# Kernel optimization log

Hardware: AMD Instinct MI355X
Metric: run time of the kernel (lower is better)

## Reference

```python
import jax, jax.numpy as jnp
import numpy as np

EMBED_DIM = 512
NUM_TYPES = 26
PER_TYPE = 128
NUM_CODES = NUM_TYPES * PER_TYPE
COMMIT = 0.25
TEMP = 0.07
N_TOKENS = 32768
SAMPLED_PER_TYPE = int(0.1 * PER_TYPE)  # 12


def _normalize(v, axis=-1):
    # matches F.normalize(p=2) with eps clamp
    return v / jnp.clip(jnp.linalg.norm(v, axis=axis, keepdims=True), 1e-12)


def setup_inputs() -> dict:
    key = jax.random.key(0)
    k1, k2, k3, k4 = jax.random.split(key, 4)
    x = jax.random.normal(k1, (N_TOKENS, EMBED_DIM), jnp.float32)
    Q = jax.random.randint(k2, (N_TOKENS,), 0, NUM_TYPES)
    initrange = 1.0 / EMBED_DIM
    emb = jax.random.uniform(k3, (NUM_CODES, EMBED_DIM), jnp.float32, -initrange, initrange)
    emb = _normalize(emb)  # mirrors _initialize_embeddings
    # deterministic stand-in for torch.randperm(num_per_type)[:sampled_num]
    perm = jax.random.permutation(k4, PER_TYPE)[:SAMPLED_PER_TYPE]
    sampled_indices = (jnp.arange(NUM_TYPES)[:, None] * PER_TYPE + perm[None, :]).reshape(-1)
    return {"x": x, "embeddings": emb, "Q": Q, "sampled_indices": sampled_indices}


def _code_indices(xn, embeddings, Q):
    # full [N, num_codes] squared distances, then select the 128-code slab of
    # each token's PTM type and argmin within it (equivalent to the per-type loop)
    d = ((xn ** 2).sum(-1, keepdims=True)
         + (embeddings ** 2).sum(-1)[None, :]
         - 2.0 * (xn @ embeddings.T))                      # [N, NUM_CODES]
    d = d.reshape(xn.shape[0], NUM_TYPES, PER_TYPE)
    d_sel = jnp.take_along_axis(d, Q[:, None, None], axis=1)[:, 0, :]  # [N, PER_TYPE]
    return jnp.argmin(d_sel, axis=1) + Q * PER_TYPE


def _uniform_loss(embeddings, sampled_indices):
    ne = _normalize(embeddings)
    se = ne[sampled_indices]                               # [S, D]
    sim = se @ se.T                                        # [S, S]
    labels = sampled_indices // PER_TYPE
    pos = (labels[None, :] == labels[:, None]).astype(jnp.float32)
    S = sampled_indices.shape[0]
    eye = jnp.eye(S, dtype=bool)
    sim = jnp.where(eye, -jnp.inf, sim)
    sim_exp = jnp.exp(sim / TEMP)                          # exp(-inf) = 0 kills diagonal
    sum_exp = sim_exp.sum(axis=1)
    pos_sum = (sim_exp * pos).sum(axis=1)
    return -jnp.log(pos_sum / sum_exp).mean()


def reference(x, embeddings, Q, sampled_indices):
    xn = _normalize(x)
    idx = _code_indices(xn, embeddings, Q)
    quantized = _normalize(embeddings[idx])
    q_latent = jnp.mean((quantized - jax.lax.stop_gradient(xn)) ** 2)
    e_latent = jnp.mean((xn - jax.lax.stop_gradient(quantized)) ** 2)
    loss = q_latent + COMMIT * e_latent
    uloss = _uniform_loss(embeddings, sampled_indices)
    out = xn + jax.lax.stop_gradient(quantized - xn)       # straight-through
    return out, loss, uloss, idx
```

## Files before the change

### kernel.cpp

```cpp
#include <hip/hip_runtime.h>
#include <math.h>

#define NTOK   32768
#define DIM    512
#define NTYPES 26
#define PT     128
#define NCODES 3328
#define NSAMP  312
#define INV_TEMP (1.0f / 0.07f)
#define MAXTILES 24

typedef __attribute__((ext_vector_type(8))) short short8;
typedef __attribute__((ext_vector_type(4))) float floatx4;

__device__ __forceinline__ void f2bf2(float f, unsigned short& h, unsigned short& l) {
    unsigned u = __float_as_uint(f);
    unsigned hb = (u + 0x7fffu + ((u >> 16) & 1u)) >> 16;
    h = (unsigned short)hb;
    float hf = __uint_as_float(hb << 16);
    float r = f - hf;
    unsigned u2 = __float_as_uint(r);
    l = (unsigned short)((u2 + 0x7fffu + ((u2 >> 16) & 1u)) >> 16);
}

__device__ __forceinline__ void cvt8(float4 a, float4 b, short8& h, short8& l) {
    union { short8 v; unsigned short u[8]; } H, L;
    f2bf2(a.x, H.u[0], L.u[0]); f2bf2(a.y, H.u[1], L.u[1]);
    f2bf2(a.z, H.u[2], L.u[2]); f2bf2(a.w, H.u[3], L.u[3]);
    f2bf2(b.x, H.u[4], L.u[4]); f2bf2(b.y, H.u[5], L.u[5]);
    f2bf2(b.z, H.u[6], L.u[6]); f2bf2(b.w, H.u[7], L.u[7]);
    h = H.v; l = L.v;
}

__device__ __forceinline__ void stage2(const unsigned short* g, unsigned short* l) {
    __builtin_amdgcn_global_load_lds((const __attribute__((address_space(1))) void*)g,
                                     (__attribute__((address_space(3))) void*)l, 16, 0, 0);
    __builtin_amdgcn_global_load_lds((const __attribute__((address_space(1))) void*)(g + 512),
                                     (__attribute__((address_space(3))) void*)(l + 512), 16, 0, 0);
}

__global__ __launch_bounds__(256) void k_emb(const float* __restrict__ emb,
                                             unsigned short* __restrict__ Bhg,
                                             unsigned short* __restrict__ Blg,
                                             float* __restrict__ sume,
                                             float* __restrict__ rinv,
                                             int* __restrict__ counts,
                                             float* __restrict__ accg) {
    int tid = threadIdx.x;
    if (blockIdx.x == 0) {
        if (tid < NTYPES) counts[tid] = 0;
        if (tid == 32) accg[0] = 0.0f;
        if (tid == 33) accg[1] = 0.0f;
    }
    int wv = tid >> 6, lane = tid & 63;
    int c = blockIdx.x * 4 + wv;
    const float4* row = (const float4*)(emb + (size_t)c * DIM);
    float4 v0 = row[lane * 2], v1 = row[lane * 2 + 1];
    float s = v0.x*v0.x + v0.y*v0.y + v0.z*v0.z + v0.w*v0.w
            + v1.x*v1.x + v1.y*v1.y + v1.z*v1.z + v1.w*v1.w;
    for (int m = 32; m; m >>= 1) s += __shfl_xor(s, m);
    if (lane == 0) {
        sume[c] = s;
        rinv[c] = 1.0f / fmaxf(sqrtf(s), 1e-12f);
    }
    union { short8 v; unsigned short u[8]; } hh, ll;
    f2bf2(v0.x, hh.u[0], ll.u[0]); f2bf2(v0.y, hh.u[1], ll.u[1]);
    f2bf2(v0.z, hh.u[2], ll.u[2]); f2bf2(v0.w, hh.u[3], ll.u[3]);
    f2bf2(v1.x, hh.u[4], ll.u[4]); f2bf2(v1.y, hh.u[5], ll.u[5]);
    f2bf2(v1.z, hh.u[6], ll.u[6]); f2bf2(v1.w, hh.u[7], ll.u[7]);
    int qq  = c >> 7;
    int n   = c & 127;
    int ni  = n >> 4, lcc = n & 15;
    int ks2 = lane >> 2, q4d = lane & 3;
    size_t dst = (size_t)qq * (PT * DIM)
               + (size_t)(((ks2 * 8 + ni) * 64 + q4d * 16 + lcc) * 8);
    *(short8*)(Bhg + dst) = hh.v;
    *(short8*)(Blg + dst) = ll.v;
}

__global__ __launch_bounds__(256) void k_hist(const int* __restrict__ Q,
                                              int* __restrict__ counts,
                                              int* __restrict__ rank) {
    __shared__ int lbin[NTYPES];
    __shared__ int lbase[NTYPES];
    int tid = threadIdx.x;
    if (tid < NTYPES) lbin[tid] = 0;
    __syncthreads();
    int t = blockIdx.x * 256 + tid;
    int qt = Q[t];
    int lr = atomicAdd(&lbin[qt], 1);
    __syncthreads();
    if (tid < NTYPES) lbase[tid] = atomicAdd(&counts[tid], lbin[tid]);
    __syncthreads();
    rank[t] = lbase[qt] + lr;
}

__global__ __launch_bounds__(256) void k_scatter(const int* __restrict__ Q,
                                                 const int* __restrict__ counts,
                                                 const int* __restrict__ rank,
                                                 int* __restrict__ order,
                                                 int* __restrict__ offsg) {
    __shared__ int offs[NTYPES];
    int tid = threadIdx.x;
    if (tid == 0) {
        int a = 0;
        for (int i = 0; i < NTYPES; i++) {
            offs[i] = a;
            if (blockIdx.x == 0) offsg[i] = a;
            a += counts[i];
        }
        if (blockIdx.x == 0) offsg[NTYPES] = a;
    }
    __syncthreads();
    int t = blockIdx.x * 256 + tid;
    order[offs[Q[t]] + rank[t]] = t;
}

#define KSTEP(S, NSTR, AC, AF, DOSTAGE)                                          \
  {                                                                              \
    __builtin_amdgcn_sched_barrier(0);                                           \
    asm volatile("s_waitcnt vmcnt(" NSTR ")" ::: "memory");                      \
    __builtin_amdgcn_s_barrier();                                                \
    __builtin_amdgcn_sched_barrier(0);                                           \
    if (DOSTAGE) {                                                               \
      stage2(bhg + ((S) + 2) * 4096 + stoff, &Bls[((S) + 2) % 3][0][ldoff]);     \
      stage2(blg + ((S) + 2) * 4096 + stoff, &Bls[((S) + 2) % 3][1][ldoff]);     \
      AF[0] = *(const float4*)(ap0 + ((S) + 2) * 32);                            \
      AF[1] = *(const float4*)(ap0 + ((S) + 2) * 32 + 4);                        \
      AF[2] = *(const float4*)(ap1 + ((S) + 2) * 32);                            \
      AF[3] = *(const float4*)(ap1 + ((S) + 2) * 32 + 4);                        \
    }                                                                            \
    __builtin_amdgcn_sched_barrier(0);                                           \
    {                                                                            \
      float4 r0a = AC[0], r0b = AC[1], r1a = AC[2], r1b = AC[3];                 \
      ps0 = fmaf(r0a.x, r0a.x, fmaf(r0a.y, r0a.y, fmaf(r0a.z, r0a.z, fmaf(r0a.w, r0a.w, ps0)))); \
      ps0 = fmaf(r0b.x, r0b.x, fmaf(r0b.y, r0b.y, fmaf(r0b.z, r0b.z, fmaf(r0b.w, r0b.w, ps0)))); \
      ps1 = fmaf(r1a.x, r1a.x, fmaf(r1a.y, r1a.y, fmaf(r1a.z, r1a.z, fmaf(r1a.w, r1a.w, ps1)))); \
      ps1 = fmaf(r1b.x, r1b.x, fmaf(r1b.y, r1b.y, fmaf(r1b.z, r1b.z, fmaf(r1b.w, r1b.w, ps1)))); \
      short8 ah0, al0, ah1, al1;                                                 \
      cvt8(r0a, r0b, ah0, al0);                                                  \
      cvt8(r1a, r1b, ah1, al1);                                                  \
      short8 bhf[4], blf[4];                                                     \
      _Pragma("unroll")                                                          \
      for (int ni = 0; ni < 4; ni++) {                                           \
        bhf[ni] = *(const short8*)&Bls[(S) % 3][0][(wn4 + ni) * 512 + lane8];    \
        blf[ni] = *(const short8*)&Bls[(S) % 3][1][(wn4 + ni) * 512 + lane8];    \
      }                                                                          \
      _Pragma("unroll")                                                          \
      for (int ni = 0; ni < 4; ni++) {                                           \
        acc[0][ni] = __builtin_amdgcn_mfma_f32_16x16x32_bf16(ah0, bhf[ni], acc[0][ni], 0, 0, 0); \
        acc[0][ni] = __builtin_amdgcn_mfma_f32_16x16x32_bf16(ah0, blf[ni], acc[0][ni], 0, 0, 0); \
        acc[0][ni] = __builtin_amdgcn_mfma_f32_16x16x32_bf16(al0, bhf[ni], acc[0][ni], 0, 0, 0); \
        acc[1][ni] = __builtin_amdgcn_mfma_f32_16x16x32_bf16(ah1, bhf[ni], acc[1][ni], 0, 0, 0); \
        acc[1][ni] = __builtin_amdgcn_mfma_f32_16x16x32_bf16(ah1, blf[ni], acc[1][ni], 0, 0, 0); \
        acc[1][ni] = __builtin_amdgcn_mfma_f32_16x16x32_bf16(al1, bhf[ni], acc[1][ni], 0, 0, 0); \
      }                                                                          \
    }                                                                            \
  }

__global__ __launch_bounds__(256, 3) void k_main(const float* __restrict__ x,
                                                 const unsigned short* __restrict__ Bhg,
                                                 const unsigned short* __restrict__ Blg,
                                                 const int* __restrict__ order,
                                                 const int* __restrict__ offsg,
                                                 const float* __restrict__ sume,
                                                 const float* __restrict__ rinv,
                                                 float* __restrict__ idxout,
                                                 float* __restrict__ accg) {
    int q = blockIdx.x;
    int tile = blockIdx.y;
    int base = offsg[q];
    int cnt = offsg[q + 1] - base;
    int tstart = tile * 64;
    if (tstart >= cnt) return;
    int nt = min(64, cnt - tstart);

    __shared__ unsigned short Bls[3][2][4096];
    __shared__ int   toks_s[64];
    __shared__ float sume_s[128];
    __shared__ float rinv_s[128];
    __shared__ float redv[64][2];
    __shared__ int   redi[64][2];

    int tid = threadIdx.x;
    int lane = tid & 63;
    int wv = tid >> 6;
    int wm = wv & 1, wn = wv >> 1;
    int lc = lane & 15, q4 = lane >> 4;
    int wn4 = wn * 4, lane8 = lane * 8;
    int stoff = wv * 1024 + lane8;
    int ldoff = wv * 1024;

    if (tid < 64) toks_s[tid] = order[base + tstart + min(tid, nt - 1)];
    if (tid < 128) {
        sume_s[tid] = sume[q * PT + tid];
        rinv_s[tid] = rinv[q * PT + tid];
    }

    int row0 = wm * 32 + lc;
    int tok0 = order[base + tstart + min(row0, nt - 1)];
    int tok1 = order[base + tstart + min(row0 + 16, nt - 1)];
    const float* ap0 = x + (size_t)tok0 * DIM + q4 * 8;
    const float* ap1 = x + (size_t)tok1 * DIM + q4 * 8;

    const unsigned short* bhg = Bhg + (size_t)q * (PT * DIM);
    const unsigned short* blg = Blg + (size_t)q * (PT * DIM);

    floatx4 acc[2][4];
#pragma unroll
    for (int mi = 0; mi < 2; mi++)
#pragma unroll
        for (int ni = 0; ni < 4; ni++)
            acc[mi][ni] = (floatx4){0.f, 0.f, 0.f, 0.f};
    float ps0 = 0.f, ps1 = 0.f;
    float4 Aa[4], Ab[4], Ac[4];

    stage2(bhg + stoff, &Bls[0][0][ldoff]);
    stage2(blg + stoff, &Bls[0][1][ldoff]);
    __builtin_amdgcn_sched_barrier(0);
    Aa[0] = *(const float4*)(ap0);      Aa[1] = *(const float4*)(ap0 + 4);
    Aa[2] = *(const float4*)(ap1);      Aa[3] = *(const float4*)(ap1 + 4);
    __builtin_amdgcn_sched_barrier(0);
    stage2(bhg + 4096 + stoff, &Bls[1][0][ldoff]);
    stage2(blg + 4096 + stoff, &Bls[1][1][ldoff]);
    __builtin_amdgcn_sched_barrier(0);
    Ab[0] = *(const float4*)(ap0 + 32); Ab[1] = *(const float4*)(ap0 + 36);
    Ab[2] = *(const float4*)(ap1 + 32); Ab[3] = *(const float4*)(ap1 + 36);

    KSTEP(0,  "8", Aa, Ac, 1)
    KSTEP(1,  "8", Ab, Aa, 1)
    KSTEP(2,  "8", Ac, Ab, 1)
    KSTEP(3,  "8", Aa, Ac, 1)
    KSTEP(4,  "8", Ab, Aa, 1)
    KSTEP(5,  "8", Ac, Ab, 1)
    KSTEP(6,  "8", Aa, Ac, 1)
    KSTEP(7,  "8", Ab, Aa, 1)
    KSTEP(8,  "8", Ac, Ab, 1)
    KSTEP(9,  "8", Aa, Ac, 1)
    KSTEP(10, "8", Ab, Aa, 1)
    KSTEP(11, "8", Ac, Ab, 1)
    KSTEP(12, "8", Aa, Ac, 1)
    KSTEP(13, "8", Ab, Aa, 1)
    KSTEP(14, "8", Ac, Ab, 0)
    KSTEP(15, "0", Aa, Ab, 0)

    ps0 += __shfl_xor(ps0, 16); ps0 += __shfl_xor(ps0, 32);
    ps1 += __shfl_xor(ps1, 16); ps1 += __shfl_xor(ps1, 32);
    float rn0 = 1.0f / fmaxf(sqrtf(ps0), 1e-12f);
    float rn1 = 1.0f / fmaxf(sqrtf(ps1), 1e-12f);

#pragma unroll
    for (int mi = 0; mi < 2; mi++) {
#pragma unroll
        for (int r = 0; r < 4; r++) {
            int rowrel = q4 * 4 + r;
            float rn = __shfl(mi == 0 ? rn0 : rn1, rowrel);
            float rn2v = -2.0f * rn;
            float bv = 1e30f; int bc = 0;
#pragma unroll
            for (int ni = 0; ni < 4; ni++) {
                int n = wn * 64 + ni * 16 + lc;
                float d = fmaf(rn2v, acc[mi][ni][r], sume_s[n]);
                if (d < bv) { bv = d; bc = n; }
            }
#pragma unroll
            for (int mk = 1; mk <= 8; mk <<= 1) {
                float ov = __shfl_xor(bv, mk);
                int oc = __shfl_xor(bc, mk);
                if (ov < bv || (ov == bv && oc < bc)) { bv = ov; bc = oc; }
            }
            int m = wm * 32 + mi * 16 + rowrel;
            if (lc == 0) { redv[m][wn] = bv; redi[m][wn] = bc; }
        }
    }
    __syncthreads();

    if (tid < 64) {
        float v0 = redv[tid][0], v1 = redv[tid][1];
        int c = (v1 < v0) ? redi[tid][1] : redi[tid][0];
        float bvv = fminf(v0, v1);
        float term = 0.0f;
        if (tid < nt) {
            idxout[toks_s[tid]] = (float)(q * PT + c);
            term = 2.0f - (sume_s[c] - bvv) * rinv_s[c];
        }
        for (int mk = 32; mk; mk >>= 1) term += __shfl_xor(term, mk);
        if (tid == 0) atomicAdd(&accg[0], term);
    }
}

__global__ __launch_bounds__(256) void k_out(const float* __restrict__ emb,
                                             const float* __restrict__ rinv,
                                             const float* __restrict__ idxf,
                                             float* __restrict__ outbuf) {
    int tid = threadIdx.x, lane = tid & 63, wv = tid >> 6;
    int tbase = blockIdx.x * 64 + wv * 16;
    int cL = 0; float rvL = 0.f;
    if (lane < 16) {
        cL = (int)idxf[tbase + lane];
        rvL = rinv[cL];
    }
    const float4* er = (const float4*)emb;
    int c0 = __shfl(cL, 0); float rv0 = __shfl(rvL, 0);
    float4 ea = er[(size_t)c0 * 128 + lane * 2];
    float4 eb = er[(size_t)c0 * 128 + lane * 2 + 1];
#pragma unroll
    for (int t = 0; t < 16; t++) {
        float4 ca = ea, cb = eb;
        float rv = rv0;
        if (t < 15) {
            int c1 = __shfl(cL, t + 1);
            rv0 = __shfl(rvL, t + 1);
            ea = er[(size_t)c1 * 128 + lane * 2];
            eb = er[(size_t)c1 * 128 + lane * 2 + 1];
        }
        float4* orow = (float4*)(outbuf + (size_t)(tbase + t) * DIM);
        orow[lane * 2]     = make_float4(ca.x * rv, ca.y * rv, ca.z * rv, ca.w * rv);
        orow[lane * 2 + 1] = make_float4(cb.x * rv, cb.y * rv, cb.z * rv, cb.w * rv);
    }
}

__global__ __launch_bounds__(256) void k_uloss(const float* __restrict__ emb,
                                               const int* __restrict__ samp,
                                               const float* __restrict__ rinv,
                                               float* __restrict__ accg) {
    __shared__ float rs[4], rp[4];
    int i = blockIdx.x;
    int tid = threadIdx.x;
    int lane = tid & 63, wv = tid >> 6;
    int ci = samp[i];
    float rvi = rinv[ci];
    int labi = ci >> 7;
    const float4* ri = (const float4*)(emb + (size_t)ci * DIM);
    float4 e0 = ri[lane * 2], e1 = ri[lane * 2 + 1];
    float sE = 0.0f, pE = 0.0f;
    for (int j0 = wv; j0 < NSAMP; j0 += 16) {
        float d[4]; int cj[4]; bool val[4];
#pragma unroll
        for (int u = 0; u < 4; u++) {
            int j = j0 + u * 4;
            val[u] = (j < NSAMP) && (j != i);
            int js = val[u] ? j : 0;
            cj[u] = samp[js];
            const float4* rj = (const float4*)(emb + (size_t)cj[u] * DIM);
            float4 f0 = rj[lane * 2], f1 = rj[lane * 2 + 1];
            d[u] = e0.x*f0.x + e0.y*f0.y + e0.z*f0.z + e0.w*f0.w
                 + e1.x*f1.x + e1.y*f1.y + e1.z*f1.z + e1.w*f1.w;
        }
#pragma unroll
        for (int mk = 32; mk; mk >>= 1)
#pragma unroll
            for (int u = 0; u < 4; u++) d[u] += __shfl_xor(d[u], mk);
#pragma unroll
        for (int u = 0; u < 4; u++) {
            float ex = val[u] ? expf(d[u] * rvi * rinv[cj[u]] * INV_TEMP) : 0.0f;
            sE += ex;
            if (val[u] && (cj[u] >> 7) == labi) pE += ex;
        }
    }
    if (lane == 0) { rs[wv] = sE; rp[wv] = pE; }
    __syncthreads();
    if (tid == 0) {
        float S = rs[0] + rs[1] + rs[2] + rs[3];
        float P = rp[0] + rp[1] + rp[2] + rp[3];
        atomicAdd(&accg[1], logf(S) - logf(P));
    }
}

__global__ void k_final(const float* __restrict__ accg, float* __restrict__ lossp) {
    lossp[0] = (1.25f / ((float)NTOK * (float)DIM)) * accg[0];
    lossp[1] = accg[1] / (float)NSAMP;
}

extern "C" void kernel_launch(void* const* d_in, const int* in_sizes, int n_in,
                              void* d_out, int out_size, void* d_ws, size_t ws_size,
                              hipStream_t stream) {
    const float* x   = (const float*)d_in[0];
    const float* emb = (const float*)d_in[1];
    const int* Q     = (const int*)d_in[2];
    const int* samp  = (const int*)d_in[3];

    float* out    = (float*)d_out;
    float* lossp  = out + (size_t)NTOK * DIM;
    float* idxout = out + (size_t)NTOK * DIM + 2;

    unsigned short* Bhg = (unsigned short*)d_ws;
    unsigned short* Blg = Bhg + (size_t)NCODES * DIM;
    float* sume  = (float*)(Blg + (size_t)NCODES * DIM);
    float* rinv  = sume + NCODES;
    int* counts  = (int*)(rinv + NCODES);
    int* offsg   = counts + NTYPES;
    int* rank    = offsg + NTYPES + 1;
    int* order   = rank + NTOK;
    float* accg  = (float*)(order + NTOK);

    k_emb<<<NCODES / 4, 256, 0, stream>>>(emb, Bhg, Blg, sume, rinv, counts, accg);
    k_hist<<<NTOK / 256, 256, 0, stream>>>(Q, counts, rank);
    k_scatter<<<NTOK / 256, 256, 0, stream>>>(Q, counts, rank, order, offsg);
    dim3 gmain(NTYPES, MAXTILES);
    k_main<<<gmain, 256, 0, stream>>>(x, Bhg, Blg, order, offsg, sume, rinv, idxout, accg);
    k_out<<<NTOK / 64, 256, 0, stream>>>(emb, rinv, idxout, out);
    k_uloss<<<NSAMP, 256, 0, stream>>>(emb, samp, rinv, accg);
    k_final<<<1, 1, 0, stream>>>(accg, lossp);
}
```

Baseline: 214.5 us.

## Fuse seven launches into three: merged preprocessing, single-block sort, merged post kernel

Embedding conversion, histogram and scatter are merged into one kernel. A dedicated 1024-thread block does the counting sort of tokens by type using wave ballots, producing a deterministic order with no global atomics. The output-gather and uniform-loss kernels are merged into one grid, and the final loss write is done by the last-finishing block through a done counter instead of a separate kernel. This cuts launch gaps and drops the rank and counts buffers. The tradeoff is that the whole 32K-token sort now runs serially in one block, which could become the critical path of the preprocessing kernel.

Result: slower. 296.0 us (+38.0%).

```diff
diff --git a/kernel.cpp b/kernel.cpp
--- a/kernel.cpp
+++ b/kernel.cpp
@@ -39,81 +39,83 @@
                                      (__attribute__((address_space(3))) void*)(l + 512), 16, 0, 0);
 }
 
-__global__ __launch_bounds__(256) void k_emb(const float* __restrict__ emb,
-                                             unsigned short* __restrict__ Bhg,
-                                             unsigned short* __restrict__ Blg,
-                                             float* __restrict__ sume,
-                                             float* __restrict__ rinv,
-                                             int* __restrict__ counts,
-                                             float* __restrict__ accg) {
+__global__ __launch_bounds__(1024) void k_pre(const float* __restrict__ emb,
+                                              const int* __restrict__ Q,
+                                              unsigned short* __restrict__ Bhg,
+                                              unsigned short* __restrict__ Blg,
+                                              float* __restrict__ sume,
+                                              float* __restrict__ rinv,
+                                              int* __restrict__ order,
+                                              int* __restrict__ offsg,
+                                              float* __restrict__ accg,
+                                              int* __restrict__ donec) {
     int tid = threadIdx.x;
-    if (blockIdx.x == 0) {
-        if (tid < NTYPES) counts[tid] = 0;
-        if (tid == 32) accg[0] = 0.0f;
-        if (tid == 33) accg[1] = 0.0f;
+    int wv = tid >> 6, lane = tid & 63;
+    if (blockIdx.x < 208) {
+        int c = blockIdx.x * 16 + wv;
+        const float4* row = (const float4*)(emb + (size_t)c * DIM);
+        float4 v0 = row[lane * 2], v1 = row[lane * 2 + 1];
+        float s = v0.x*v0.x + v0.y*v0.y + v0.z*v0.z + v0.w*v0.w
+                + v1.x*v1.x + v1.y*v1.y + v1.z*v1.z + v1.w*v1.w;
+        for (int m = 32; m; m >>= 1) s += __shfl_xor(s, m);
+        if (lane == 0) {
+            sume[c] = s;
+            rinv[c] = 1.0f / fmaxf(sqrtf(s), 1e-12f);
+        }
+        union { short8 v; unsigned short u[8]; } hh, ll;
+        f2bf2(v0.x, hh.u[0], ll.u[0]); f2bf2(v0.y, hh.u[1], ll.u[1]);
+        f2bf2(v0.z, hh.u[2], ll.u[2]); f2bf2(v0.w, hh.u[3], ll.u[3]);
+        f2bf2(v1.x, hh.u[4], ll.u[4]); f2bf2(v1.y, hh.u[5], ll.u[5]);
+        f2bf2(v1.z, hh.u[6], ll.u[6]); f2bf2(v1.w, hh.u[7], ll.u[7]);
+        int qq  = c >> 7;
+        int n   = c & 127;
+        int ni  = n >> 4, lcc = n & 15;
+        int ks2 = lane >> 2, q4d = lane & 3;
+        size_t dst = (size_t)qq * (PT * DIM)
+                   + (size_t)(((ks2 * 8 + ni) * 64 + q4d * 16 + lcc) * 8);
+        *(short8*)(Bhg + dst) = hh.v;
+        *(short8*)(Blg + dst) = ll.v;
+    } else {
+        __shared__ int wcnt[16][NTYPES];
+        __shared__ int wbase[16][NTYPES];
+        if (tid == 0) { accg[0] = 0.0f; accg[1] = 0.0f; *donec = 0; }
+        int cw = 0;
+        for (int chunk = 0; chunk < 32; chunk++) {
+            int ti = wv * 2048 + chunk * 64 + lane;
+            int q = Q[ti];
+#pragma unroll
+            for (int t = 0; t < NTYPES; t++) {
+                unsigned long long m = __ballot(q == t);
+                if (lane == t) cw += (int)__popcll(m);
+            }
+        }
+        if (lane < NTYPES) wcnt[wv][lane] = cw;
+        __syncthreads();
+        if (tid == 0) {
+            int a = 0;
+            for (int t = 0; t < NTYPES; t++) {
+                offsg[t] = a;
+                int s = 0;
+                for (int w = 0; w < 16; w++) { wbase[w][t] = a + s; s += wcnt[w][t]; }
+                a += s;
+            }
+            offsg[NTYPES] = a;
+        }
+        __syncthreads();
+        int rb = (lane < NTYPES) ? wbase[wv][lane] : 0;
+        unsigned long long ltm = (1ULL << lane) - 1ULL;
+        for (int chunk = 0; chunk < 32; chunk++) {
+            int ti = wv * 2048 + chunk * 64 + lane;
+            int q = Q[ti];
+#pragma unroll
+            for (int t = 0; t < NTYPES; t++) {
+                unsigned long long m = __ballot(q == t);
+                int b = __shfl(rb, t);
+                if (q == t) order[b + (int)__popcll(m & ltm)] = ti;
+                if (lane == t) rb += (int)__popcll(m);
+            }
+        }
     }
-    int wv = tid >> 6, lane = tid & 63;
-    int c = blockIdx.x * 4 + wv;
-    const float4* row = (const float4*)(emb + (size_t)c * DIM);
-    float4 v0 = row[lane * 2], v1 = row[lane * 2 + 1];
-    float s = v0.x*v0.x + v0.y*v0.y + v0.z*v0.z + v0.w*v0.w
-            + v1.x*v1.x + v1.y*v1.y + v1.z*v1.z + v1.w*v1.w;
-    for (int m = 32; m; m >>= 1) s += __shfl_xor(s, m);
-    if (lane == 0) {
-        sume[c] = s;
-        rinv[c] = 1.0f / fmaxf(sqrtf(s), 1e-12f);
-    }
-    union { short8 v; unsigned short u[8]; } hh, ll;
-    f2bf2(v0.x, hh.u[0], ll.u[0]); f2bf2(v0.y, hh.u[1], ll.u[1]);
-    f2bf2(v0.z, hh.u[2], ll.u[2]); f2bf2(v0.w, hh.u[3], ll.u[3]);
-    f2bf2(v1.x, hh.u[4], ll.u[4]); f2bf2(v1.y, hh.u[5], ll.u[5]);
-    f2bf2(v1.z, hh.u[6], ll.u[6]); f2bf2(v1.w, hh.u[7], ll.u[7]);
-    int qq  = c >> 7;
-    int n   = c & 127;
-    int ni  = n >> 4, lcc = n & 15;
-    int ks2 = lane >> 2, q4d = lane & 3;
-    size_t dst = (size_t)qq * (PT * DIM)
-               + (size_t)(((ks2 * 8 + ni) * 64 + q4d * 16 + lcc) * 8);
-    *(short8*)(Bhg + dst) = hh.v;
-    *(short8*)(Blg + dst) = ll.v;
-}
-
-__global__ __launch_bounds__(256) void k_hist(const int* __restrict__ Q,
-                                              int* __restrict__ counts,
-                                              int* __restrict__ rank) {
-    __shared__ int lbin[NTYPES];
-    __shared__ int lbase[NTYPES];
-    int tid = threadIdx.x;
-    if (tid < NTYPES) lbin[tid] = 0;
-    __syncthreads();
-    int t = blockIdx.x * 256 + tid;
-    int qt = Q[t];
-    int lr = atomicAdd(&lbin[qt], 1);
-    __syncthreads();
-    if (tid < NTYPES) lbase[tid] = atomicAdd(&counts[tid], lbin[tid]);
-    __syncthreads();
-    rank[t] = lbase[qt] + lr;
-}
-
-__global__ __launch_bounds__(256) void k_scatter(const int* __restrict__ Q,
-                                                 const int* __restrict__ counts,
-                                                 const int* __restrict__ rank,
-                                                 int* __restrict__ order,
-                                                 int* __restrict__ offsg) {
-    __shared__ int offs[NTYPES];
-    int tid = threadIdx.x;
-    if (tid == 0) {
-        int a = 0;
-        for (int i = 0; i < NTYPES; i++) {
-            offs[i] = a;
-            if (blockIdx.x == 0) offsg[i] = a;
-            a += counts[i];
-        }
-        if (blockIdx.x == 0) offsg[NTYPES] = a;
-    }
-    __syncthreads();
-    int t = blockIdx.x * 256 + tid;
-    order[offs[Q[t]] + rank[t]] = t;
 }
 
 #define KSTEP(S, NSTR, AC, AF, DOSTAGE)                                          \
@@ -289,87 +291,91 @@
     }
 }
 
-__global__ __launch_bounds__(256) void k_out(const float* __restrict__ emb,
-                                             const float* __restrict__ rinv,
-                                             const float* __restrict__ idxf,
-                                             float* __restrict__ outbuf) {
+__global__ __launch_bounds__(256) void k_post(const float* __restrict__ emb,
+                                              const float* __restrict__ rinv,
+                                              const float* __restrict__ idxf,
+                                              float* __restrict__ outbuf,
+                                              const int* __restrict__ samp,
+                                              float* __restrict__ accg,
+                                              int* __restrict__ donec,
+                                              float* __restrict__ lossp) {
+    int bid = blockIdx.x;
     int tid = threadIdx.x, lane = tid & 63, wv = tid >> 6;
-    int tbase = blockIdx.x * 64 + wv * 16;
-    int cL = 0; float rvL = 0.f;
-    if (lane < 16) {
-        cL = (int)idxf[tbase + lane];
-        rvL = rinv[cL];
+    if (bid < NTOK / 64) {
+        int tbase = bid * 64 + wv * 16;
+        int cL = 0; float rvL = 0.f;
+        if (lane < 16) {
+            cL = (int)idxf[tbase + lane];
+            rvL = rinv[cL];
+        }
+        const float4* er = (const float4*)emb;
+        int c0 = __shfl(cL, 0); float rv0 = __shfl(rvL, 0);
+        float4 ea = er[(size_t)c0 * 128 + lane * 2];
+        float4 eb = er[(size_t)c0 * 128 + lane * 2 + 1];
+#pragma unroll
+        for (int t = 0; t < 16; t++) {
+            float4 ca = ea, cb = eb;
+            float rv = rv0;
+            if (t < 15) {
+                int c1 = __shfl(cL, t + 1);
+                rv0 = __shfl(rvL, t + 1);
+                ea = er[(size_t)c1 * 128 + lane * 2];
+                eb = er[(size_t)c1 * 128 + lane * 2 + 1];
+            }
+            float4* orow = (float4*)(outbuf + (size_t)(tbase + t) * DIM);
+            orow[lane * 2]     = make_float4(ca.x * rv, ca.y * rv, ca.z * rv, ca.w * rv);
+            orow[lane * 2 + 1] = make_float4(cb.x * rv, cb.y * rv, cb.z * rv, cb.w * rv);
+        }
+    } else {
+        __shared__ float rs[4], rp[4];
+        int i = bid - NTOK / 64;
+        int ci = samp[i];
+        float rvi = rinv[ci];
+        int labi = ci >> 7;
+        const float4* ri = (const float4*)(emb + (size_t)ci * DIM);
+        float4 e0 = ri[lane * 2], e1 = ri[lane * 2 + 1];
+        float sE = 0.0f, pE = 0.0f;
+        for (int j0 = wv; j0 < NSAMP; j0 += 16) {
+            float d[4]; int cj[4]; bool val[4];
+#pragma unroll
+            for (int u = 0; u < 4; u++) {
+                int j = j0 + u * 4;
+                val[u] = (j < NSAMP) && (j != i);
+                int js = val[u] ? j : 0;
+                cj[u] = samp[js];
+                const float4* rj = (const float4*)(emb + (size_t)cj[u] * DIM);
+                float4 f0 = rj[lane * 2], f1 = rj[lane * 2 + 1];
+                d[u] = e0.x*f0.x + e0.y*f0.y + e0.z*f0.z + e0.w*f0.w
+                     + e1.x*f1.x + e1.y*f1.y + e1.z*f1.z + e1.w*f1.w;
+            }
+#pragma unroll
+            for (int mk = 32; mk; mk >>= 1)
+#pragma unroll
+                for (int u = 0; u < 4; u++) d[u] += __shfl_xor(d[u], mk);
+#pragma unroll
+            for (int u = 0; u < 4; u++) {
+                float ex = val[u] ? expf(d[u] * rvi * rinv[cj[u]] * INV_TEMP) : 0.0f;
+                sE += ex;
+                if (val[u] && (cj[u] >> 7) == labi) pE += ex;
+            }
+        }
+        if (lane == 0) { rs[wv] = sE; rp[wv] = pE; }
+        __syncthreads();
+        if (tid == 0) {
+            float S = rs[0] + rs[1] + rs[2] + rs[3];
+            float P = rp[0] + rp[1] + rp[2] + rp[3];
+            atomicAdd(&accg[1], logf(S) - logf(P));
+            __threadfence();
+            int old = atomicAdd(donec, 1);
+            if (old == NSAMP - 1) {
+                __threadfence();
+                float a0 = atomicAdd(&accg[0], 0.0f);
+                float a1 = atomicAdd(&accg[1], 0.0f);
+                lossp[0] = (1.25f / ((float)NTOK * (float)DIM)) * a0;
+                lossp[1] = a1 / (float)NSAMP;
+            }
+        }
     }
-    const float4* er = (const float4*)emb;
-    int c0 = __shfl(cL, 0); float rv0 = __shfl(rvL, 0);
-    float4 ea = er[(size_t)c0 * 128 + lane * 2];
-    float4 eb = er[(size_t)c0 * 128 + lane * 2 + 1];
-#pragma unroll
-    for (int t = 0; t < 16; t++) {
-        float4 ca = ea, cb = eb;
-        float rv = rv0;
-        if (t < 15) {
-            int c1 = __shfl(cL, t + 1);
-            rv0 = __shfl(rvL, t + 1);
-            ea = er[(size_t)c1 * 128 + lane * 2];
-            eb = er[(size_t)c1 * 128 + lane * 2 + 1];
-        }
-        float4* orow = (float4*)(outbuf + (size_t)(tbase + t) * DIM);
-        orow[lane * 2]     = make_float4(ca.x * rv, ca.y * rv, ca.z * rv, ca.w * rv);
-        orow[lane * 2 + 1] = make_float4(cb.x * rv, cb.y * rv, cb.z * rv, cb.w * rv);
-    }
-}
-
-__global__ __launch_bounds__(256) void k_uloss(const float* __restrict__ emb,
-                                               const int* __restrict__ samp,
-                                               const float* __restrict__ rinv,
-                                               float* __restrict__ accg) {
-    __shared__ float rs[4], rp[4];
-    int i = blockIdx.x;
-    int tid = threadIdx.x;
-    int lane = tid & 63, wv = tid >> 6;
-    int ci = samp[i];
-    float rvi = rinv[ci];
-    int labi = ci >> 7;
-    const float4* ri = (const float4*)(emb + (size_t)ci * DIM);
-    float4 e0 = ri[lane * 2], e1 = ri[lane * 2 + 1];
-    float sE = 0.0f, pE = 0.0f;
-    for (int j0 = wv; j0 < NSAMP; j0 += 16) {
-        float d[4]; int cj[4]; bool val[4];
-#pragma unroll
-        for (int u = 0; u < 4; u++) {
-            int j = j0 + u * 4;
-            val[u] = (j < NSAMP) && (j != i);
-            int js = val[u] ? j : 0;
-            cj[u] = samp[js];
-            const float4* rj = (const float4*)(emb + (size_t)cj[u] * DIM);
-            float4 f0 = rj[lane * 2], f1 = rj[lane * 2 + 1];
-            d[u] = e0.x*f0.x + e0.y*f0.y + e0.z*f0.z + e0.w*f0.w
-                 + e1.x*f1.x + e1.y*f1.y + e1.z*f1.z + e1.w*f1.w;
-        }
-#pragma unroll
-        for (int mk = 32; mk; mk >>= 1)
-#pragma unroll
-            for (int u = 0; u < 4; u++) d[u] += __shfl_xor(d[u], mk);
-#pragma unroll
-        for (int u = 0; u < 4; u++) {
-            float ex = val[u] ? expf(d[u] * rvi * rinv[cj[u]] * INV_TEMP) : 0.0f;
-            sE += ex;
-            if (val[u] && (cj[u] >> 7) == labi) pE += ex;
-        }
-    }
-    if (lane == 0) { rs[wv] = sE; rp[wv] = pE; }
-    __syncthreads();
-    if (tid == 0) {
-        float S = rs[0] + rs[1] + rs[2] + rs[3];
-        float P = rp[0] + rp[1] + rp[2] + rp[3];
-        atomicAdd(&accg[1], logf(S) - logf(P));
-    }
-}
-
-__global__ void k_final(const float* __restrict__ accg, float* __restrict__ lossp) {
-    lossp[0] = (1.25f / ((float)NTOK * (float)DIM)) * accg[0];
-    lossp[1] = accg[1] / (float)NSAMP;
 }
 
 extern "C" void kernel_launch(void* const* d_in, const int* in_sizes, int n_in,
@@ -388,18 +394,13 @@
     unsigned short* Blg = Bhg + (size_t)NCODES * DIM;
     float* sume  = (float*)(Blg + (size_t)NCODES * DIM);
     float* rinv  = sume + NCODES;
-    int* counts  = (int*)(rinv + NCODES);
-    int* offsg   = counts + NTYPES;
-    int* rank    = offsg + NTYPES + 1;
-    int* order   = rank + NTOK;
+    int* offsg   = (int*)(rinv + NCODES);
+    int* order   = offsg + NTYPES + 1;
     float* accg  = (float*)(order + NTOK);
-
-    k_emb<<<NCODES / 4, 256, 0, stream>>>(emb, Bhg, Blg, sume, rinv, counts, accg);
-    k_hist<<<NTOK / 256, 256, 0, stream>>>(Q, counts, rank);
-    k_scatter<<<NTOK / 256, 256, 0, stream>>>(Q, counts, rank, order, offsg);
+    int* donec   = (int*)(accg + 2);
+
+    k_pre<<<209, 1024, 0, stream>>>(emb, Q, Bhg, Blg, sume, rinv, order, offsg, accg, donec);
     dim3 gmain(NTYPES, MAXTILES);
     k_main<<<gmain, 256, 0, stream>>>(x, Bhg, Blg, order, offsg, sume, rinv, idxout, accg);
-    k_out<<<NTOK / 64, 256, 0, stream>>>(emb, rinv, idxout, out);
-    k_uloss<<<NSAMP, 256, 0, stream>>>(emb, samp, rinv, accg);
-    k_final<<<1, 1, 0, stream>>>(accg, lossp);
-}
+    k_post<<<NTOK / 64 + NSAMP, 256, 0, stream>>>(emb, rinv, idxout, out, samp, accg, donec, lossp);
+}
```
